# Optimization experiments

Hardware: AMD Instinct MI355X
Metric: run time of the kernel (lower is better)

Reference implementation:

```python
import jax, jax.numpy as jnp
import numpy as np

D_MODEL = 1024
N_HEADS = 16
D_V = D_MODEL // N_HEADS  # 64


def setup_inputs() -> dict:
    key = jax.random.key(0)
    k1, k2, k3, k4, k5, k6 = jax.random.split(key, 6)
    N, L = 2, 2048
    return {
        "queries": jax.random.normal(k1, (N, L, D_MODEL), jnp.float32),
        "keys": jax.random.normal(k2, (N, L, D_MODEL), jnp.float32),
        "values": jax.random.normal(k3, (N, L, D_MODEL), jnp.float32),
        # key-padding mask, 0 = masked out (broadcast over heads and queries)
        "mask": jax.random.randint(k4, (N, 1, 1, L), 0, 2).astype(jnp.int32),
        # torch nn.Linear(d_model, d_model): weight [out, in], bias [out]
        "fc_w": jax.random.normal(k5, (D_MODEL, D_MODEL), jnp.float32) / np.sqrt(D_MODEL).astype(np.float32),
        "fc_b": jax.random.normal(k6, (D_MODEL,), jnp.float32) * 0.01,
    }


def reference(queries, keys, values, mask, fc_w, fc_b):
    N, Lq, _ = queries.shape
    Lk = keys.shape[1]
    # NOTE: the source defines Q/K/V Linear layers but never applies them in forward.
    q = queries.reshape(N, Lq, N_HEADS, D_V).transpose(0, 2, 1, 3)  # [N,H,Lq,Dv]
    k = keys.reshape(N, Lk, N_HEADS, D_V)                            # [N,Lk,H,Dv]
    v = values.reshape(N, Lk, N_HEADS, D_V)                          # [N,Lk,H,Dv]
    energy = jnp.einsum('nhqd,nkhd->nhqk', q, k)                     # QK^T
    energy = jnp.where(mask == 0, -jnp.inf, energy)                  # masked_fill
    # faithful to source: scale by sqrt(d_model), applied after masking
    attn = jax.nn.softmax(energy / jnp.sqrt(jnp.float32(D_MODEL)), axis=-1)
    out = jnp.einsum('nhqk,nkhd->nqhd', attn, v).reshape(N, Lq, N_HEADS * D_V)
    return out @ fc_w.T + fc_b
```

## Files before the change

### kernel.cpp

```cpp
#include <hip/hip_runtime.h>
#include <hip/hip_bf16.h>

#define SEQL 2048
#define DMODEL 1024

typedef short bf16x8 __attribute__((ext_vector_type(8)));
typedef short bf16x4 __attribute__((ext_vector_type(4)));
typedef float f32x4 __attribute__((ext_vector_type(4)));
typedef unsigned short u16;

__device__ __forceinline__ u16 f2bf(float f) {
    union { float f; unsigned u; } v; v.f = f;
    unsigned r = v.u + 0x7FFFu + ((v.u >> 16) & 1u);
    return (u16)(r >> 16);
}

__device__ __forceinline__ void async16(u16* lds, const u16* g) {
    __builtin_amdgcn_global_load_lds(
        (const __attribute__((address_space(1))) unsigned int*)g,
        (__attribute__((address_space(3))) unsigned int*)lds,
        16, 0, 0);
}


#define TSTR 72

__global__ __launch_bounds__(256) void pack_all(
    const float* __restrict__ kg, const float* __restrict__ wg,
    const float* __restrict__ vg, const int* __restrict__ mg,
    u16* __restrict__ kb, u16* __restrict__ wb, u16* __restrict__ vtb,
    float* __restrict__ maskf)
{
    __shared__ __align__(16) u16 T[64 * TSTR];
    const int b = blockIdx.x, t = threadIdx.x;
    u16 o[8];
    if (b < 2048) {
        const int e0 = (b * 256 + t) * 8;
        const int n = e0 >> 21;
        const int s = (e0 >> 10) & 2047;
        const int dm = e0 & 1023, h = dm >> 6, d0 = dm & 63;
        const float4 x0 = *(const float4*)(kg + e0);
        const float4 x1 = *(const float4*)(kg + e0 + 4);
        o[0]=f2bf(x0.x); o[1]=f2bf(x0.y); o[2]=f2bf(x0.z); o[3]=f2bf(x0.w);
        o[4]=f2bf(x1.x); o[5]=f2bf(x1.y); o[6]=f2bf(x1.z); o[7]=f2bf(x1.w);
        const int kt = s >> 6, st = (s >> 4) & 3, m = s & 15;
        const int f = d0 >> 5, qd = (d0 >> 3) & 3;
        u16* dst = kb + ((size_t)((n * 16 + h) * 32 + kt)) * 4096
                      + (st * 2 + f) * 512 + (m + 16 * qd) * 8;
        *(bf16x8*)dst = *(bf16x8*)o;
    } else if (b < 2560) {
        const int e0 = ((b - 2048) * 256 + t) * 8;
        const int col = e0 >> 10, k0 = e0 & 1023;
        const float4 x0 = *(const float4*)(wg + e0);
        const float4 x1 = *(const float4*)(wg + e0 + 4);
        o[0]=f2bf(x0.x); o[1]=f2bf(x0.y); o[2]=f2bf(x0.z); o[3]=f2bf(x0.w);
        o[4]=f2bf(x1.x); o[5]=f2bf(x1.y); o[6]=f2bf(x1.z); o[7]=f2bf(x1.w);
        const int cb = col >> 6, cj = (col >> 4) & 3, m = col & 15;
        const int kt = k0 >> 6, f = (k0 >> 5) & 1, qd = (k0 >> 3) & 3;
        u16* dst = wb + ((size_t)((cb * 16 + kt) * 8 + cj * 2 + f)) * 512
                      + (m + 16 * qd) * 8;
        *(bf16x8*)dst = *(bf16x8*)o;
    } else if (b < 3584) {
        const int bb = b - 2560;
        const int kt = bb & 31, h = (bb >> 5) & 15, n = bb >> 9;
        {
            const int s = t >> 2, d0 = (t & 3) * 16;
            const float* src = vg + ((size_t)(n * SEQL + kt * 64 + s) * DMODEL) + h * 64 + d0;
            u16 w16[16];
            #pragma unroll
            for (int j = 0; j < 16; ++j) w16[j] = f2bf(src[j]);
            *(bf16x8*)&T[s * TSTR + d0]     = *(bf16x8*)&w16[0];
            *(bf16x8*)&T[s * TSTR + d0 + 8] = *(bf16x8*)&w16[8];
        }
        __syncthreads();
        {
            const int d = t >> 2, k0 = (t & 3) * 16;
            u16 w16[16];
            #pragma unroll
            for (int j = 0; j < 16; ++j) w16[j] = T[(k0 + j) * TSTR + d];
            const int t4 = d >> 4, dr = d & 15;
            u16* base = vtb + ((size_t)((n * 16 + h) * 32 + kt)) * 4096;
            #pragma unroll
            for (int g = 0; g < 2; ++g) {
                const int key0 = k0 + g * 8;
                const int kk = key0 >> 5, qk = (key0 >> 3) & 3;
                *(bf16x8*)(base + (t4 * 2 + kk) * 512 + (dr + 16 * qk) * 8)
                    = *(bf16x8*)&w16[g * 8];
            }
        }
    } else {
        #pragma unroll
        for (int i = 0; i < 16; ++i) {
            const int idx = t * 16 + i;
            maskf[idx] = mg[idx] ? 0.0f : -1.0e5f;
        }
    }
}

#define OSPLIT 4194304
#define LSPLIT 65536

template<int NSPLIT>
__global__ __launch_bounds__(256) void attn_kernel(
    const float* __restrict__ qg, const u16* __restrict__ kb,
    const u16* __restrict__ vtb, const float* __restrict__ maskf,
    u16* __restrict__ xb, float* __restrict__ opart, float* __restrict__ lpart)
{
    __shared__ __align__(16) u16 SM[16384];
    u16* const K_lds = SM;
    u16* const V_lds = SM + 4096;
    u16* const P_lds = SM + 8192;

    const int blk = blockIdx.x;
    const int qblk = blk & 15;
    const int h = (blk >> 4) & 15;
    const int n = (blk >> 8) & 1;
    const int split = blk >> 9;
    const int tid = threadIdx.x;
    const int wave = tid >> 6, lane = tid & 63;
    const int lrow = lane & 15, quad = lane >> 4;
    const int q0 = qblk * 128;

    bf16x8 qf[2][2];
    #pragma unroll
    for (int qi = 0; qi < 2; ++qi) {
        const float* qp = qg + ((size_t)(n * SEQL + q0 + wave * 32 + qi * 16 + lrow) * DMODEL) + h * 64 + quad * 8;
        #pragma unroll
        for (int f = 0; f < 2; ++f) {
            const float4 a = *(const float4*)(qp + f * 32);
            const float4 c = *(const float4*)(qp + f * 32 + 4);
            u16* dst = (u16*)&qf[qi][f];
            dst[0]=f2bf(a.x); dst[1]=f2bf(a.y); dst[2]=f2bf(a.z); dst[3]=f2bf(a.w);
            dst[4]=f2bf(c.x); dst[5]=f2bf(c.y); dst[6]=f2bf(c.z); dst[7]=f2bf(c.w);
        }
    }

    bf16x8 onesf;
    #pragma unroll
    for (int j = 0; j < 8; ++j) ((u16*)&onesf)[j] = 0x3F80;

    f32x4 oacc[2][4];
    f32x4 lacc[2];
    #pragma unroll
    for (int qi = 0; qi < 2; ++qi) {
        lacc[qi] = (f32x4){0.f, 0.f, 0.f, 0.f};
        #pragma unroll
        for (int t4 = 0; t4 < 4; ++t4) oacc[qi][t4] = (f32x4){0.f, 0.f, 0.f, 0.f};
    }

    const u16* ksrc0 = kb  + ((size_t)(n * 16 + h)) * 131072;
    const u16* vsrc0 = vtb + ((size_t)(n * 16 + h)) * 131072;
    const float* mrow = maskf + n * SEQL;

    const int ktlo = split * (32 / NSPLIT);
    const int kthi = ktlo + (32 / NSPLIT);

    for (int kt = ktlo; kt < kthi; ++kt) {
        __syncthreads();
        {
            const u16* ks = ksrc0 + (size_t)kt * 4096;
            const u16* vs = vsrc0 + (size_t)kt * 4096;
            #pragma unroll
            for (int i = 0; i < 2; ++i) {
                const int ch = tid + i * 256;
                async16(&K_lds[ch * 8], ks + ch * 8);
                async16(&V_lds[ch * 8], vs + ch * 8);
            }
        }
        __syncthreads();

        #pragma unroll
        for (int st = 0; st < 4; ++st) {
            const bf16x8 kf0 = *(const bf16x8*)&K_lds[(st * 2 + 0) * 512 + lane * 8];
            const bf16x8 kf1 = *(const bf16x8*)&K_lds[(st * 2 + 1) * 512 + lane * 8];
            const f32x4 mv = *(const f32x4*)&mrow[kt * 64 + st * 16 + quad * 4];
            const int kk = st >> 1;
            const int qk = (st & 1) * 2 + (quad >> 1);
            const int j0 = (quad & 1) * 4;
            #pragma unroll
            for (int qi = 0; qi < 2; ++qi) {
                f32x4 sa = (f32x4){0.f, 0.f, 0.f, 0.f};
                sa = __builtin_amdgcn_mfma_f32_16x16x32_bf16(kf0, qf[qi][0], sa, 0, 0, 0);
                sa = __builtin_amdgcn_mfma_f32_16x16x32_bf16(kf1, qf[qi][1], sa, 0, 0, 0);
                float e0v = __expf(fmaf(sa[0], 0.03125f, mv[0]));
                float e1v = __expf(fmaf(sa[1], 0.03125f, mv[1]));
                float e2v = __expf(fmaf(sa[2], 0.03125f, mv[2]));
                float e3v = __expf(fmaf(sa[3], 0.03125f, mv[3]));
                __hip_bfloat162 h0 = __float22bfloat162_rn(make_float2(e0v, e1v));
                __hip_bfloat162 h1 = __float22bfloat162_rn(make_float2(e2v, e3v));
                union { unsigned u[2]; bf16x4 v; } pk;
                pk.u[0] = *(unsigned*)&h0;
                pk.u[1] = *(unsigned*)&h1;
                *(bf16x4*)&P_lds[wave * 2048 + (qi * 2 + kk) * 512 + (lrow + 16 * qk) * 8 + j0] = pk.v;
            }
        }
        asm volatile("s_waitcnt lgkmcnt(0)" ::: "memory");

        bf16x8 vf[4][2];
        #pragma unroll
        for (int t4 = 0; t4 < 4; ++t4) {
            vf[t4][0] = *(const bf16x8*)&V_lds[(t4 * 2 + 0) * 512 + lane * 8];
            vf[t4][1] = *(const bf16x8*)&V_lds[(t4 * 2 + 1) * 512 + lane * 8];
        }
        #pragma unroll
        for (int qi = 0; qi < 2; ++qi) {
            const bf16x8 pf0 = *(const bf16x8*)&P_lds[wave * 2048 + (qi * 2 + 0) * 512 + lane * 8];
            const bf16x8 pf1 = *(const bf16x8*)&P_lds[wave * 2048 + (qi * 2 + 1) * 512 + lane * 8];
            lacc[qi] = __builtin_amdgcn_mfma_f32_16x16x32_bf16(pf0, onesf, lacc[qi], 0, 0, 0);
            lacc[qi] = __builtin_amdgcn_mfma_f32_16x16x32_bf16(pf1, onesf, lacc[qi], 0, 0, 0);
            #pragma unroll
            for (int t4 = 0; t4 < 4; ++t4) {
                oacc[qi][t4] = __builtin_amdgcn_mfma_f32_16x16x32_bf16(pf0, vf[t4][0], oacc[qi][t4], 0, 0, 0);
                oacc[qi][t4] = __builtin_amdgcn_mfma_f32_16x16x32_bf16(pf1, vf[t4][1], oacc[qi][t4], 0, 0, 0);
            }
        }
    }

    if (NSPLIT == 1) {
        #pragma unroll
        for (int qi = 0; qi < 2; ++qi)
            #pragma unroll
            for (int r = 0; r < 4; ++r) {
                const float rinv = 1.0f / lacc[qi][r];
                const int row = n * SEQL + q0 + wave * 32 + qi * 16 + quad * 4 + r;
                const int rb = row >> 7, rt = (row >> 4) & 7, m = row & 15;
                #pragma unroll
                for (int t4 = 0; t4 < 4; ++t4) {
                    const int f = t4 >> 1;
                    const int qd = (t4 & 1) * 2 + (lrow >> 3);
                    xb[((size_t)((rb * 16 + h) * 16 + rt * 2 + f)) * 512
                       + (m + 16 * qd) * 8 + (lrow & 7)] = f2bf(oacc[qi][t4][r] * rinv);
                }
            }
    } else {
        #pragma unroll
        for (int qi = 0; qi < 2; ++qi) {
            #pragma unroll
            for (int r = 0; r < 4; ++r) {
                const int q = q0 + wave * 32 + qi * 16 + quad * 4 + r;
                float* op = opart + (size_t)split * OSPLIT + (size_t)(n * SEQL + q) * DMODEL + h * 64 + lrow;
                #pragma unroll
                for (int t4 = 0; t4 < 4; ++t4)
                    op[t4 * 16] = oacc[qi][t4][r];
                if (lrow == 0)
                    lpart[split * LSPLIT + (n * SEQL + q) * 16 + h] = lacc[qi][r];
            }
        }
    }
}

template<int NSPLIT>
__global__ __launch_bounds__(256) void reduce_norm(
    const float* __restrict__ opart, const float* __restrict__ lpart,
    u16* __restrict__ xb)
{
    const int gid = blockIdx.x * 256 + threadIdx.x;
    const int e0 = gid * 8;
    const int row = e0 >> 10, k0 = e0 & 1023, h = k0 >> 6;
    float lsum = 0.f;
    #pragma unroll
    for (int s = 0; s < NSPLIT; ++s) lsum += lpart[s * LSPLIT + row * 16 + h];
    const float rinv = 1.0f / lsum;
    float a[8] = {0.f,0.f,0.f,0.f,0.f,0.f,0.f,0.f};
    #pragma unroll
    for (int s = 0; s < NSPLIT; ++s) {
        const float4 x0 = *(const float4*)(opart + (size_t)s * OSPLIT + e0);
        const float4 x1 = *(const float4*)(opart + (size_t)s * OSPLIT + e0 + 4);
        a[0]+=x0.x; a[1]+=x0.y; a[2]+=x0.z; a[3]+=x0.w;
        a[4]+=x1.x; a[5]+=x1.y; a[6]+=x1.z; a[7]+=x1.w;
    }
    u16 o[8];
    #pragma unroll
    for (int j = 0; j < 8; ++j) o[j] = f2bf(a[j] * rinv);
    const int rb = row >> 7, rt = (row >> 4) & 7, m = row & 15;
    const int kt = k0 >> 6, f = (k0 >> 5) & 1, qd = (k0 >> 3) & 3;
    *(bf16x8*)(xb + ((size_t)((rb * 16 + kt) * 16 + rt * 2 + f)) * 512
                  + (m + 16 * qd) * 8) = *(bf16x8*)o;
}

__global__ __launch_bounds__(256) void fc_kernel(
    const u16* __restrict__ xb, const u16* __restrict__ wb,
    const float* __restrict__ bias, float* __restrict__ out)
{
    __shared__ __align__(16) u16 SM[12288];
    u16* const X_lds = SM;
    u16* const W_lds = SM + 8192;

    const int blk = blockIdx.x;
    const int cb = blk & 15, rb = blk >> 4;
    const int tid = threadIdx.x;
    const int wave = tid >> 6, lane = tid & 63;
    const int lrow = lane & 15, quad = lane >> 4;

    f32x4 acc[2][4];
    #pragma unroll
    for (int ri = 0; ri < 2; ++ri)
        #pragma unroll
        for (int cj = 0; cj < 4; ++cj) acc[ri][cj] = (f32x4){0.f, 0.f, 0.f, 0.f};

    for (int kt = 0; kt < 16; ++kt) {
        __syncthreads();
        {
            const u16* xs = xb + ((size_t)(rb * 16 + kt)) * 8192;
            const u16* ws = wb + ((size_t)(cb * 16 + kt)) * 4096;
            #pragma unroll
            for (int i = 0; i < 4; ++i) {
                const int ch = tid + i * 256;
                async16(&X_lds[ch * 8], xs + ch * 8);
            }
            #pragma unroll
            for (int i = 0; i < 2; ++i) {
                const int ch = tid + i * 256;
                async16(&W_lds[ch * 8], ws + ch * 8);
            }
        }
        __syncthreads();

        bf16x8 af[2][2];
        #pragma unroll
        for (int ri = 0; ri < 2; ++ri) {
            af[ri][0] = *(const bf16x8*)&X_lds[((wave * 2 + ri) * 2 + 0) * 512 + lane * 8];
            af[ri][1] = *(const bf16x8*)&X_lds[((wave * 2 + ri) * 2 + 1) * 512 + lane * 8];
        }
        #pragma unroll
        for (int cj = 0; cj < 4; ++cj) {
            const bf16x8 bf0 = *(const bf16x8*)&W_lds[(cj * 2 + 0) * 512 + lane * 8];
            const bf16x8 bf1 = *(const bf16x8*)&W_lds[(cj * 2 + 1) * 512 + lane * 8];
            #pragma unroll
            for (int ri = 0; ri < 2; ++ri) {
                acc[ri][cj] = __builtin_amdgcn_mfma_f32_16x16x32_bf16(af[ri][0], bf0, acc[ri][cj], 0, 0, 0);
                acc[ri][cj] = __builtin_amdgcn_mfma_f32_16x16x32_bf16(af[ri][1], bf1, acc[ri][cj], 0, 0, 0);
            }
        }
    }

    const int row0 = rb * 128, col0 = cb * 64;
    #pragma unroll
    for (int ri = 0; ri < 2; ++ri)
        #pragma unroll
        for (int cj = 0; cj < 4; ++cj) {
            const int col = col0 + cj * 16 + lrow;
            const float bv = bias[col];
            #pragma unroll
            for (int r = 0; r < 4; ++r)
                out[(size_t)(row0 + wave * 32 + ri * 16 + quad * 4 + r) * DMODEL + col] = acc[ri][cj][r] + bv;
        }
}

extern "C" void kernel_launch(void* const* d_in, const int* in_sizes, int n_in,
                              void* d_out, int out_size, void* d_ws, size_t ws_size,
                              hipStream_t stream) {
    const float* q   = (const float*)d_in[0];
    const float* k   = (const float*)d_in[1];
    const float* v   = (const float*)d_in[2];
    const int*   m   = (const int*)d_in[3];
    const float* fcw = (const float*)d_in[4];
    const float* fcb = (const float*)d_in[5];
    float* out = (float*)d_out;

    char* ws = (char*)d_ws;
    u16*   kbuf  = (u16*)(ws);
    u16*   vtbuf = (u16*)(ws + (8u  << 20));
    u16*   wbuf  = (u16*)(ws + (16u << 20));
    u16*   xbuf  = (u16*)(ws + (18u << 20));
    float* maskf = (float*)(ws + (26u << 20));
    float* opart = (float*)(ws + (27u << 20));
    float* lpart = (float*)(ws + (59u << 20));
    const bool split2 = ws_size >= (60u << 20);

    pack_all<<<dim3(3585), dim3(256), 0, stream>>>(k, fcw, v, m, kbuf, wbuf, vtbuf, maskf);
    if (split2) {
        attn_kernel<2><<<dim3(1024), dim3(256), 0, stream>>>(q, kbuf, vtbuf, maskf, xbuf, opart, lpart);
        reduce_norm<2><<<dim3(2048), dim3(256), 0, stream>>>(opart, lpart, xbuf);
    } else {
        attn_kernel<1><<<dim3(512), dim3(256), 0, stream>>>(q, kbuf, vtbuf, maskf, xbuf, opart, lpart);
    }
    fc_kernel<<<dim3(512), dim3(256), 0, stream>>>(xbuf, wbuf, fcb, out);
}
```

Baseline: 179.0 us.

## Load K/V and GEMM operands directly from global memory into registers, bypassing LDS

Both the attention kernel and the output projection kernel stop staging K/V and X/W tiles through shared memory with async global-to-LDS copies and block barriers. Each wave now loads its fragments straight from global memory into registers, since the pre-packed layout already matches the MFMA fragment order. This removes two __syncthreads per tile iteration and shrinks LDS usage, which can raise occupancy. The cost is that all four waves now fetch the same K/V or W data, multiplying L2/L1 traffic and exposing global load latency without explicit prefetch.

```diff
diff --git a/kernel.cpp b/kernel.cpp
--- a/kernel.cpp
+++ b/kernel.cpp
@@ -13,13 +13,6 @@
     union { float f; unsigned u; } v; v.f = f;
     unsigned r = v.u + 0x7FFFu + ((v.u >> 16) & 1u);
     return (u16)(r >> 16);
-}
-
-__device__ __forceinline__ void async16(u16* lds, const u16* g) {
-    __builtin_amdgcn_global_load_lds(
-        (const __attribute__((address_space(1))) unsigned int*)g,
-        (__attribute__((address_space(3))) unsigned int*)lds,
-        16, 0, 0);
 }
 
 
@@ -106,10 +99,7 @@
     const u16* __restrict__ vtb, const float* __restrict__ maskf,
     u16* __restrict__ xb, float* __restrict__ opart, float* __restrict__ lpart)
 {
-    __shared__ __align__(16) u16 SM[16384];
-    u16* const K_lds = SM;
-    u16* const V_lds = SM + 4096;
-    u16* const P_lds = SM + 8192;
+    __shared__ __align__(16) u16 P_lds[4 * 2048];
 
     const int blk = blockIdx.x;
     const int qblk = blk & 15;
@@ -148,31 +138,31 @@
         for (int t4 = 0; t4 < 4; ++t4) oacc[qi][t4] = (f32x4){0.f, 0.f, 0.f, 0.f};
     }
 
-    const u16* ksrc0 = kb  + ((size_t)(n * 16 + h)) * 131072;
-    const u16* vsrc0 = vtb + ((size_t)(n * 16 + h)) * 131072;
+    const u16* ksrc0 = kb  + ((size_t)(n * 16 + h)) * 131072 + lane * 8;
+    const u16* vsrc0 = vtb + ((size_t)(n * 16 + h)) * 131072 + lane * 8;
     const float* mrow = maskf + n * SEQL;
 
     const int ktlo = split * (32 / NSPLIT);
     const int kthi = ktlo + (32 / NSPLIT);
 
     for (int kt = ktlo; kt < kthi; ++kt) {
-        __syncthreads();
-        {
-            const u16* ks = ksrc0 + (size_t)kt * 4096;
-            const u16* vs = vsrc0 + (size_t)kt * 4096;
-            #pragma unroll
-            for (int i = 0; i < 2; ++i) {
-                const int ch = tid + i * 256;
-                async16(&K_lds[ch * 8], ks + ch * 8);
-                async16(&V_lds[ch * 8], vs + ch * 8);
-            }
-        }
-        __syncthreads();
-
+        const u16* kbase = ksrc0 + (size_t)kt * 4096;
+        const u16* vbase = vsrc0 + (size_t)kt * 4096;
+
+        bf16x8 kf[4][2], vf[4][2];
         #pragma unroll
         for (int st = 0; st < 4; ++st) {
-            const bf16x8 kf0 = *(const bf16x8*)&K_lds[(st * 2 + 0) * 512 + lane * 8];
-            const bf16x8 kf1 = *(const bf16x8*)&K_lds[(st * 2 + 1) * 512 + lane * 8];
+            kf[st][0] = *(const bf16x8*)(kbase + (st * 2 + 0) * 512);
+            kf[st][1] = *(const bf16x8*)(kbase + (st * 2 + 1) * 512);
+        }
+        #pragma unroll
+        for (int t4 = 0; t4 < 4; ++t4) {
+            vf[t4][0] = *(const bf16x8*)(vbase + (t4 * 2 + 0) * 512);
+            vf[t4][1] = *(const bf16x8*)(vbase + (t4 * 2 + 1) * 512);
+        }
+
+        #pragma unroll
+        for (int st = 0; st < 4; ++st) {
             const f32x4 mv = *(const f32x4*)&mrow[kt * 64 + st * 16 + quad * 4];
             const int kk = st >> 1;
             const int qk = (st & 1) * 2 + (quad >> 1);
@@ -180,8 +170,8 @@
             #pragma unroll
             for (int qi = 0; qi < 2; ++qi) {
                 f32x4 sa = (f32x4){0.f, 0.f, 0.f, 0.f};
-                sa = __builtin_amdgcn_mfma_f32_16x16x32_bf16(kf0, qf[qi][0], sa, 0, 0, 0);
-                sa = __builtin_amdgcn_mfma_f32_16x16x32_bf16(kf1, qf[qi][1], sa, 0, 0, 0);
+                sa = __builtin_amdgcn_mfma_f32_16x16x32_bf16(kf[st][0], qf[qi][0], sa, 0, 0, 0);
+                sa = __builtin_amdgcn_mfma_f32_16x16x32_bf16(kf[st][1], qf[qi][1], sa, 0, 0, 0);
                 float e0v = __expf(fmaf(sa[0], 0.03125f, mv[0]));
                 float e1v = __expf(fmaf(sa[1], 0.03125f, mv[1]));
                 float e2v = __expf(fmaf(sa[2], 0.03125f, mv[2]));
@@ -196,12 +186,6 @@
         }
         asm volatile("s_waitcnt lgkmcnt(0)" ::: "memory");
 
-        bf16x8 vf[4][2];
-        #pragma unroll
-        for (int t4 = 0; t4 < 4; ++t4) {
-            vf[t4][0] = *(const bf16x8*)&V_lds[(t4 * 2 + 0) * 512 + lane * 8];
-            vf[t4][1] = *(const bf16x8*)&V_lds[(t4 * 2 + 1) * 512 + lane * 8];
-        }
         #pragma unroll
         for (int qi = 0; qi < 2; ++qi) {
             const bf16x8 pf0 = *(const bf16x8*)&P_lds[wave * 2048 + (qi * 2 + 0) * 512 + lane * 8];
@@ -282,10 +266,6 @@
     const u16* __restrict__ xb, const u16* __restrict__ wb,
     const float* __restrict__ bias, float* __restrict__ out)
 {
-    __shared__ __align__(16) u16 SM[12288];
-    u16* const X_lds = SM;
-    u16* const W_lds = SM + 8192;
-
     const int blk = blockIdx.x;
     const int cb = blk & 15, rb = blk >> 4;
     const int tid = threadIdx.x;
@@ -298,40 +278,30 @@
         #pragma unroll
         for (int cj = 0; cj < 4; ++cj) acc[ri][cj] = (f32x4){0.f, 0.f, 0.f, 0.f};
 
+    const u16* xs0 = xb + ((size_t)rb * 16) * 8192 + lane * 8;
+    const u16* ws0 = wb + ((size_t)cb * 16) * 4096 + lane * 8;
+
     for (int kt = 0; kt < 16; ++kt) {
-        __syncthreads();
-        {
-            const u16* xs = xb + ((size_t)(rb * 16 + kt)) * 8192;
-            const u16* ws = wb + ((size_t)(cb * 16 + kt)) * 4096;
-            #pragma unroll
-            for (int i = 0; i < 4; ++i) {
-                const int ch = tid + i * 256;
-                async16(&X_lds[ch * 8], xs + ch * 8);
-            }
-            #pragma unroll
-            for (int i = 0; i < 2; ++i) {
-                const int ch = tid + i * 256;
-                async16(&W_lds[ch * 8], ws + ch * 8);
-            }
-        }
-        __syncthreads();
-
-        bf16x8 af[2][2];
+        const u16* xs = xs0 + (size_t)kt * 8192;
+        const u16* ws = ws0 + (size_t)kt * 4096;
+        bf16x8 af[2][2], bf[4][2];
         #pragma unroll
         for (int ri = 0; ri < 2; ++ri) {
-            af[ri][0] = *(const bf16x8*)&X_lds[((wave * 2 + ri) * 2 + 0) * 512 + lane * 8];
-            af[ri][1] = *(const bf16x8*)&X_lds[((wave * 2 + ri) * 2 + 1) * 512 + lane * 8];
+            af[ri][0] = *(const bf16x8*)(xs + ((wave * 2 + ri) * 2 + 0) * 512);
+            af[ri][1] = *(const bf16x8*)(xs + ((wave * 2 + ri) * 2 + 1) * 512);
         }
         #pragma unroll
         for (int cj = 0; cj < 4; ++cj) {
-            const bf16x8 bf0 = *(const bf16x8*)&W_lds[(cj * 2 + 0) * 512 + lane * 8];
-            const bf16x8 bf1 = *(const bf16x8*)&W_lds[(cj * 2 + 1) * 512 + lane * 8];
+            bf[cj][0] = *(const bf16x8*)(ws + (cj * 2 + 0) * 512);
+            bf[cj][1] = *(const bf16x8*)(ws + (cj * 2 + 1) * 512);
+        }
+        #pragma unroll
+        for (int cj = 0; cj < 4; ++cj)
             #pragma unroll
             for (int ri = 0; ri < 2; ++ri) {
-                acc[ri][cj] = __builtin_amdgcn_mfma_f32_16x16x32_bf16(af[ri][0], bf0, acc[ri][cj], 0, 0, 0);
-                acc[ri][cj] = __builtin_amdgcn_mfma_f32_16x16x32_bf16(af[ri][1], bf1, acc[ri][cj], 0, 0, 0);
-            }
-        }
+                acc[ri][cj] = __builtin_amdgcn_mfma_f32_16x16x32_bf16(af[ri][0], bf[cj][0], acc[ri][cj], 0, 0, 0);
+                acc[ri][cj] = __builtin_amdgcn_mfma_f32_16x16x32_bf16(af[ri][1], bf[cj][1], acc[ri][cj], 0, 0, 0);
+            }
     }
 
     const int row0 = rb * 128, col0 = cb * 64;
```

New measurement: 210.8 us. 17.7% more time.
